# Kernel optimization log

Measured on AMD Instinct MI355X. Metric: run time of the kernel, lower is better.

The kernel has to match this reference:

```python
import jax, jax.numpy as jnp
import numpy as np


def _chain_edges(n):
    # bidirectional chain edges + self loops (PyG GATConv add_self_loops=True default)
    src = np.concatenate([np.arange(n - 1), np.arange(1, n), np.arange(n)])
    dst = np.concatenate([np.arange(1, n), np.arange(n - 1), np.arange(n)])
    return jnp.asarray(src), jnp.asarray(dst)


def _gat(x, W, a_src, a_dst, bias, src, dst, n, heads, ch, concat):
    # x: [B, n, Fin]; PyG GATConv v1 math (lin has no bias, bias added post-agg)
    B = x.shape[0]
    xh = (x @ W).reshape(B, n, heads, ch)  # [B,n,h,c]
    es = jnp.einsum('bnhc,hc->bnh', xh, a_src)
    ed = jnp.einsum('bnhc,hc->bnh', xh, a_dst)
    e = jax.nn.leaky_relu(es[:, src] + ed[:, dst], 0.2)  # [B,E,h]
    e = jnp.moveaxis(e, 1, 0)                            # [E,B,h]
    m = jax.ops.segment_max(e, dst, num_segments=n)      # scatter-softmax over incoming edges
    w = jnp.exp(e - m[dst])
    denom = jax.ops.segment_sum(w, dst, num_segments=n)
    alpha = w / denom[dst]                               # [E,B,h]
    msgs = alpha[..., None] * jnp.moveaxis(xh[:, src], 1, 0)  # [E,B,h,c]
    out = jnp.moveaxis(jax.ops.segment_sum(msgs, dst, num_segments=n), 0, 1)  # [B,n,h,c]
    out = out.reshape(B, n, heads * ch) if concat else out.mean(axis=2)
    return out + bias


def _mlp(x, w1, b1, w2, b2, w3, b3):
    h = jax.nn.leaky_relu(x @ w1 + b1, 0.01)
    h = jax.nn.leaky_relu(h @ w2 + b2, 0.01)
    return h @ w3 + b3


def setup_inputs() -> dict:
    key = jax.random.key(0)
    ks = jax.random.split(key, 21)
    B, n, d_state, hid, da = 2048, 50, 64, 128, 4
    r = lambda k, shp, s: (jax.random.normal(k, shp, dtype=jnp.float32) * s)
    return {
        'state': r(ks[0], (B, n, d_state), 1.0),
        'W1': r(ks[1], (d_state, 2 * hid), 0.1), 'att_src1': r(ks[2], (2, hid), 0.1),
        'att_dst1': r(ks[3], (2, hid), 0.1), 'b1': r(ks[4], (2 * hid,), 0.02),
        'W2': r(ks[5], (2 * hid, hid), 0.1), 'att_src2': r(ks[6], (1, hid), 0.1),
        'att_dst2': r(ks[7], (1, hid), 0.1), 'b2': r(ks[8], (hid,), 0.02),
        'aw1': r(ks[9], (hid, 128), 0.1), 'ab1': r(ks[10], (128,), 0.02),
        'aw2': r(ks[11], (128, 128), 0.1), 'ab2': r(ks[12], (128,), 0.02),
        'aw3': r(ks[13], (128, da), 0.1), 'ab3': r(ks[14], (da,), 0.02),
        'vw1': r(ks[15], (hid, 128), 0.1), 'vb1': r(ks[16], (128,), 0.02),
        'vw2': r(ks[17], (128, 128), 0.1), 'vb2': r(ks[18], (128,), 0.02),
        'vw3': r(ks[19], (128, 1), 0.1), 'vb3': r(ks[20], (1,), 0.02),
    }


def reference(state, W1, att_src1, att_dst1, b1, W2, att_src2, att_dst2, b2,
              aw1, ab1, aw2, ab2, aw3, ab3, vw1, vb1, vw2, vb2, vw3, vb3):
    B, n, _ = state.shape
    src, dst = _chain_edges(n)
    x = jax.nn.gelu(_gat(state, W1, att_src1, att_dst1, b1, src, dst, n, 2, 128, True), approximate=False)
    x = jax.nn.gelu(_gat(x, W2, att_src2, att_dst2, b2, src, dst, n, 1, 128, False), approximate=False)
    graph_emb = x.mean(axis=1)                      # global_mean_pool over chain nodes
    value = _mlp(graph_emb, vw1, vb1, vw2, vb2, vw3, vb3)   # [B,1]
    mean = _mlp(x, aw1, ab1, aw2, ab2, aw3, ab3).reshape(B, -1)  # [B, n*d_action]
    return mean, value
```

## Files before the change

### kernel.cpp

```cpp
#include <hip/hip_runtime.h>

#define DI __device__ __forceinline__

typedef unsigned int uint32;
typedef unsigned short u16;
typedef __attribute__((ext_vector_type(8))) short s8v;
typedef __attribute__((ext_vector_type(4))) float f4v;

DI float lrelu(float x, float s){ return x > 0.f ? x : s*x; }
DI u16 f2bu(float f){ uint32 u = __float_as_uint(f); return (u16)((u + 0x7FFFu + ((u>>16)&1u)) >> 16); }
DI float fastrcp(float x){ float r; asm("v_rcp_f32 %0, %1" : "=v"(r) : "v"(x)); return r; }

DI float gelu_f(float x){
  const float z = fabsf(x) * 0.70710678118654752f;
  const float t = fastrcp(1.f + 0.3275911f*z);
  float p = 1.061405429f;
  p = p*t - 1.453152027f;
  p = p*t + 1.421413741f;
  p = p*t - 0.284496736f;
  p = p*t + 0.254829592f;
  p = p*t;
  const float e = __expf(-z*z);
  float er = 1.f - p*e;
  er = copysignf(er, x);
  return 0.5f*x*(1.f + er);
}

DI f4v mfma16(s8v a, s8v b, f4v c){
  return __builtin_amdgcn_mfma_f32_16x16x32_bf16(a, b, c, 0, 0, 0);
}

constexpr int NNODE = 50;
constexpr int NT = 512;
constexpr int SCS = 134;

constexpr int WS1  = 0;
constexpr int WS2  = 18432;
constexpr int WSA1 = 55296;
constexpr int WSA2 = 71680;
constexpr int WSA3 = 88064;
constexpr int WSTOT= 90112;

__global__ __launch_bounds__(256)
void ac_prep(const float* __restrict__ w1, const float* __restrict__ as1, const float* __restrict__ ad1,
             const float* __restrict__ w2, const float* __restrict__ as2, const float* __restrict__ ad2,
             const float* __restrict__ aw1, const float* __restrict__ aw2, const float* __restrict__ aw3,
             u16* __restrict__ ws)
{
  const int T1 = 2*144*64, T2 = 144*256, T3 = 128*128;
  for (int t = blockIdx.x*blockDim.x + threadIdx.x; t < WSTOT; t += gridDim.x*blockDim.x){
    float v; int o;
    if (t < T1){
      int h = t / 9216, r = t - h*9216, n = r>>6, k = r&63;
      if (n < 128) v = w1[k*256 + h*128 + n];
      else if (n < 130){
        const float* av = ((n==129) ? ad1 : as1) + h*128;
        const float* wr = w1 + k*256 + h*128;
        float s = 0.f;
        for (int c=0;c<128;++c) s += wr[c]*av[c];
        v = s;
      } else v = 0.f;
      o = WS1 + h*9216 + n*64 + k;
    } else if (t < T1+T2){
      int j = t - T1, n = j>>8, k = j&255;
      if (n < 128) v = w2[k*128 + n];
      else if (n < 130){
        const float* av = (n==129) ? ad2 : as2;
        const float* wr = w2 + k*128;
        float s = 0.f;
        for (int c=0;c<128;++c) s += wr[c]*av[c];
        v = s;
      } else v = 0.f;
      o = WS2 + n*256 + k;
    } else if (t < T1+T2+T3){
      int j = t - T1 - T2, n = j>>7, k = j&127;
      v = aw1[k*128 + n];
      o = WSA1 + n*128 + k;
    } else if (t < T1+T2+2*T3){
      int j = t - T1 - T2 - T3, n = j>>7, k = j&127;
      v = aw2[k*128 + n];
      o = WSA2 + n*128 + k;
    } else {
      int j = t - T1 - T2 - 2*T3, m = j>>7, k = j&127;
      v = (m < 4) ? aw3[k*4 + m] : 0.f;
      o = WSA3 + m*128 + k;
    }
    ws[o] = f2bu(v);
  }
}


__global__ __launch_bounds__(NT)
void ac_main(const float* __restrict__ state,
             const float* __restrict__ b1, const float* __restrict__ b2,
             const float* __restrict__ ab1, const float* __restrict__ ab2,
             const float* __restrict__ ab3,
             const float* __restrict__ vw1, const float* __restrict__ vb1,
             const float* __restrict__ vw2, const float* __restrict__ vb2,
             const float* __restrict__ vw3, const float* __restrict__ vb3,
             const u16* __restrict__ ws,
             float* __restrict__ out_mean, float* __restrict__ out_val)
{
  __shared__ __align__(16) float sm[18816];
  float* sc   = sm;
  u16*   pAb  = (u16*)(sm + 8576);
  u16*   pAb2 = pAb + 8192;
  u16*   pAs  = (u16*)(sm + 16768);
  float* geb4 = sm + 16768;
  float* geb  = sm + 17280;
  float* vh1  = sm + 17408;

  const int tid = threadIdx.x, b = blockIdx.x;
  const int wid = tid>>6, l15 = tid&15, g = (tid>>4)&3;

  {
    const float4* xb4 = (const float4*)(state + (size_t)b * (NNODE*64));
    for (int t = tid; t < 800; t += NT){
      float4 v = xb4[t];
      int i = t>>4, k0 = (t&15)*4;
      ushort4 u;
      u.x = f2bu(v.x); u.y = f2bu(v.y); u.z = f2bu(v.z); u.w = f2bu(v.w);
      *(ushort4*)(pAs + i*64 + (k0 ^ ((i&7)<<3))) = u;
    }
    for (int t = tid; t < 224; t += NT){
      int i = 50 + (t>>4), k0 = (t&15)*4;
      *(ushort4*)(pAs + i*64 + (k0 ^ ((i&7)<<3))) = (ushort4){0,0,0,0};
    }
  }
  __syncthreads();

  {
    s8v aS[4][2];
    #pragma unroll
    for (int mt=0;mt<4;++mt)
      #pragma unroll
      for (int ks=0;ks<2;++ks){
        int row = mt*16 + l15, c = ks*32 + g*8;
        aS[mt][ks] = *(const s8v*)(pAs + row*64 + (c ^ ((row&7)<<3)));
      }

    for (int h=0; h<2; ++h){
      for (int nt = wid; nt < 9; nt += 8){
        f4v acc[4];
        #pragma unroll
        for (int mt=0;mt<4;++mt) acc[mt] = (f4v){0.f,0.f,0.f,0.f};
        #pragma unroll
        for (int ks=0;ks<2;++ks){
          s8v bf = *(const s8v*)(ws + WS1 + h*9216 + (nt*16 + l15)*64 + ks*32 + g*8);
          #pragma unroll
          for (int mt=0;mt<4;++mt) acc[mt] = mfma16(aS[mt][ks], bf, acc[mt]);
        }
        const int col = nt*16 + l15;
        if (col < 130){
          #pragma unroll
          for (int mt=0;mt<4;++mt){
            const int r0 = mt*16 + g*4;
            #pragma unroll
            for (int r=0;r<4;++r) sc[(r0+r)*SCS + col] = acc[mt][r];
          }
        }
      }
      __syncthreads();

      {
        const int i = tid & 63;
        if (i < NNODE){
          const float edi = sc[i*SCS + 129];
          const float eS = __expf(lrelu(sc[i*SCS + 128] + edi, 0.2f));
          const float eL = (i > 0)       ? __expf(lrelu(sc[(i-1)*SCS + 128] + edi, 0.2f)) : 0.f;
          const float eR = (i < NNODE-1) ? __expf(lrelu(sc[(i+1)*SCS + 128] + edi, 0.2f)) : 0.f;
          const float rs = fastrcp(eL + eS + eR);
          sc[i*SCS + 130] = eL*rs;
          sc[i*SCS + 131] = eS*rs;
          sc[i*SCS + 132] = eR*rs;
        }
      }
      {
        const int q = tid>>7, j = tid&127, jj = h*128 + j;
        const int i0 = q*13, i1 = (i0+13 < NNODE) ? i0+13 : NNODE;
        const float bj = b1[jj];
        float pv  = (i0 > 0) ? sc[(i0-1)*SCS + j] : 0.f;
        float cur = sc[i0*SCS + j];
        #pragma unroll 4
        for (int i = i0; i < i1; ++i){
          const float nx = (i < NNODE-1) ? sc[(i+1)*SCS + j] : 0.f;
          const float wL = sc[i*SCS + 130], wS = sc[i*SCS + 131], wR = sc[i*SCS + 132];
          const float v = gelu_f(wL*pv + wS*cur + wR*nx + bj);
          pAb[i*256 + (jj ^ ((i&7)<<3))] = f2bu(v);
          pv = cur; cur = nx;
        }
      }
      __syncthreads();
    }
  }

  for (int nt = wid; nt < 9; nt += 8){
    f4v acc[4];
    #pragma unroll
    for (int mt=0;mt<4;++mt) acc[mt] = (f4v){0.f,0.f,0.f,0.f};
    #pragma unroll
    for (int ks=0;ks<8;++ks){
      s8v bf = *(const s8v*)(ws + WS2 + (nt*16 + l15)*256 + ks*32 + g*8);
      #pragma unroll
      for (int mt=0;mt<4;++mt){
        const int row = mt*16 + l15, c = ks*32 + g*8;
        s8v a = *(const s8v*)(pAb + row*256 + (c ^ ((row&7)<<3)));
        acc[mt] = mfma16(a, bf, acc[mt]);
      }
    }
    const int col = nt*16 + l15;
    if (col < 130){
      #pragma unroll
      for (int mt=0;mt<4;++mt){
        const int r0 = mt*16 + g*4;
        #pragma unroll
        for (int r=0;r<4;++r) sc[(r0+r)*SCS + col] = acc[mt][r];
      }
    }
  }
  __syncthreads();

  {
    const int i = tid & 63;
    if (i < NNODE){
      const float edi = sc[i*SCS + 129];
      const float eS = __expf(lrelu(sc[i*SCS + 128] + edi, 0.2f));
      const float eL = (i > 0)       ? __expf(lrelu(sc[(i-1)*SCS + 128] + edi, 0.2f)) : 0.f;
      const float eR = (i < NNODE-1) ? __expf(lrelu(sc[(i+1)*SCS + 128] + edi, 0.2f)) : 0.f;
      const float rs = fastrcp(eL + eS + eR);
      sc[i*SCS + 130] = eL*rs;
      sc[i*SCS + 131] = eS*rs;
      sc[i*SCS + 132] = eR*rs;
    }
  }
  {
    const int q = tid>>7, j = tid&127;
    const int i0 = q*13, i1 = (i0+13 < NNODE) ? i0+13 : NNODE;
    const float bj = b2[j];
    float ps = 0.f;
    float pv  = (i0 > 0) ? sc[(i0-1)*SCS + j] : 0.f;
    float cur = sc[i0*SCS + j];
    #pragma unroll 4
    for (int i = i0; i < i1; ++i){
      const float nx = (i < NNODE-1) ? sc[(i+1)*SCS + j] : 0.f;
      const float wL = sc[i*SCS + 130], wS = sc[i*SCS + 131], wR = sc[i*SCS + 132];
      const float v = gelu_f(wL*pv + wS*cur + wR*nx + bj);
      pAb[i*128 + (j ^ ((i&7)<<3))] = f2bu(v);
      ps += v;
      pv = cur; cur = nx;
    }
    geb4[q*128 + j] = ps;
  }
  __syncthreads();

  {
    const int nt = wid;
    f4v acc[4];
    #pragma unroll
    for (int mt=0;mt<4;++mt) acc[mt] = (f4v){0.f,0.f,0.f,0.f};
    #pragma unroll
    for (int ks=0;ks<4;++ks){
      s8v bf = *(const s8v*)(ws + WSA1 + (nt*16 + l15)*128 + ks*32 + g*8);
      #pragma unroll
      for (int mt=0;mt<4;++mt){
        const int row = mt*16 + l15, c = ks*32 + g*8;
        s8v a = *(const s8v*)(pAb + row*128 + (c ^ ((row&7)<<3)));
        acc[mt] = mfma16(a, bf, acc[mt]);
      }
    }
    const int col = nt*16 + l15;
    const float bj = ab1[col];
    #pragma unroll
    for (int mt=0;mt<4;++mt){
      #pragma unroll
      for (int r=0;r<4;++r){
        const int row = mt*16 + g*4 + r;
        const float v = lrelu(acc[mt][r] + bj, 0.01f);
        pAb2[row*128 + (col ^ ((row&7)<<3))] = f2bu(v);
      }
    }
    if (tid < 128)
      geb[tid] = (geb4[tid] + geb4[128+tid] + geb4[256+tid] + geb4[384+tid]) * 0.02f;
  }
  __syncthreads();

  {
    const int nt = wid;
    f4v acc[4];
    #pragma unroll
    for (int mt=0;mt<4;++mt) acc[mt] = (f4v){0.f,0.f,0.f,0.f};
    #pragma unroll
    for (int ks=0;ks<4;++ks){
      s8v bf = *(const s8v*)(ws + WSA2 + (nt*16 + l15)*128 + ks*32 + g*8);
      #pragma unroll
      for (int mt=0;mt<4;++mt){
        const int row = mt*16 + l15, c = ks*32 + g*8;
        s8v a = *(const s8v*)(pAb2 + row*128 + (c ^ ((row&7)<<3)));
        acc[mt] = mfma16(a, bf, acc[mt]);
      }
    }
    const int col = nt*16 + l15;
    const float bj = ab2[col];
    #pragma unroll
    for (int mt=0;mt<4;++mt){
      #pragma unroll
      for (int r=0;r<4;++r){
        const int row = mt*16 + g*4 + r;
        const float v = lrelu(acc[mt][r] + bj, 0.01f);
        pAb[row*128 + (col ^ ((row&7)<<3))] = f2bu(v);
      }
    }
  }
  __syncthreads();

  if (wid < 4){
    const int mt = wid;
    f4v acc = (f4v){0.f,0.f,0.f,0.f};
    #pragma unroll
    for (int ks=0;ks<4;++ks){
      s8v bf = *(const s8v*)(ws + WSA3 + l15*128 + ks*32 + g*8);
      const int row = mt*16 + l15, c = ks*32 + g*8;
      s8v a = *(const s8v*)(pAb + row*128 + (c ^ ((row&7)<<3)));
      acc = mfma16(a, bf, acc);
    }
    if (l15 < 4){
      const float bj = ab3[l15];
      #pragma unroll
      for (int r=0;r<4;++r){
        const int row = mt*16 + g*4 + r;
        if (row < NNODE) out_mean[(size_t)b*200 + row*4 + l15] = acc[r] + bj;
      }
    }
  } else if (wid == 4){
    const int j = tid & 63;
    float a0=0.f, a1=0.f;
    #pragma unroll 4
    for (int k=0;k<128;++k){
      const float gk = geb[k];
      a0 += gk*vw1[k*128 + j];
      a1 += gk*vw1[k*128 + j + 64];
    }
    vh1[j]      = lrelu(a0 + vb1[j],    0.01f);
    vh1[j + 64] = lrelu(a1 + vb1[j+64], 0.01f);
    asm volatile("s_waitcnt lgkmcnt(0)" ::: "memory");
    __builtin_amdgcn_sched_barrier(0);
    float c0=0.f, c1=0.f;
    #pragma unroll 4
    for (int k=0;k<128;++k){
      const float hk = vh1[k];
      c0 += hk*vw2[k*128 + j];
      c1 += hk*vw2[k*128 + j + 64];
    }
    const float va = lrelu(c0 + vb2[j],    0.01f);
    const float vb = lrelu(c1 + vb2[j+64], 0.01f);
    float p = va*vw3[j] + vb*vw3[j+64];
    #pragma unroll
    for (int off=32; off>0; off>>=1) p += __shfl_down(p, off);
    if (j == 0) out_val[b] = p + vb3[0];
  }
}

extern "C" void kernel_launch(void* const* d_in, const int* in_sizes, int n_in,
                              void* d_out, int out_size, void* d_ws, size_t ws_size,
                              hipStream_t stream)
{
  const float* state = (const float*)d_in[0];
  const float* w1    = (const float*)d_in[1];
  const float* as1   = (const float*)d_in[2];
  const float* ad1   = (const float*)d_in[3];
  const float* b1_   = (const float*)d_in[4];
  const float* w2    = (const float*)d_in[5];
  const float* as2   = (const float*)d_in[6];
  const float* ad2   = (const float*)d_in[7];
  const float* b2_   = (const float*)d_in[8];
  const float* aw1   = (const float*)d_in[9];
  const float* ab1   = (const float*)d_in[10];
  const float* aw2   = (const float*)d_in[11];
  const float* ab2   = (const float*)d_in[12];
  const float* aw3   = (const float*)d_in[13];
  const float* ab3   = (const float*)d_in[14];
  const float* vw1   = (const float*)d_in[15];
  const float* vb1   = (const float*)d_in[16];
  const float* vw2   = (const float*)d_in[17];
  const float* vb2   = (const float*)d_in[18];
  const float* vw3   = (const float*)d_in[19];
  const float* vb3   = (const float*)d_in[20];

  const int B = in_sizes[0] / (NNODE * 64);
  float* out_mean = (float*)d_out;
  float* out_val  = out_mean + (size_t)B * 200;
  u16* ws = (u16*)d_ws;

  ac_prep<<<128, 256, 0, stream>>>(w1, as1, ad1, w2, as2, ad2, aw1, aw2, aw3, ws);
  ac_main<<<B, NT, 0, stream>>>(state, b1_, b2_, ab1, ab2, ab3,
                                vw1, vb1, vw2, vb2, vw3, vb3,
                                ws, out_mean, out_val);
}
```

Baseline: 145.8 us.

## Shrink LDS footprint with bf16 scratch and load inputs directly into MFMA fragments

The fp32 GEMM scratch buffer becomes a bf16 buffer, and the attention scalars and softmax weights move into small separate arrays. This cuts shared memory from about 75KB to about 54KB so more blocks fit per CU, and launch_bounds now asks for 6 waves per SIMD. The state input is loaded from global memory straight into register A-fragments, dropping the LDS staging pass and one barrier. Software bf16 rounding is replaced by the hardware v_cvt_pk_bf16_f32 instruction. Storing the intermediate projections in bf16 adds rounding error before aggregation, and the occupancy hint may raise register pressure.

```diff
diff --git a/kernel.cpp b/kernel.cpp
--- a/kernel.cpp
+++ b/kernel.cpp
@@ -8,8 +8,11 @@
 typedef __attribute__((ext_vector_type(4))) float f4v;
 
 DI float lrelu(float x, float s){ return x > 0.f ? x : s*x; }
+DI float fastrcp(float x){ float r; asm("v_rcp_f32 %0, %1" : "=v"(r) : "v"(x)); return r; }
+DI u16 f2b16(float x){ uint32 r; asm("v_cvt_pk_bf16_f32 %0, %1, %1" : "=v"(r) : "v"(x)); return (u16)r; }
+DI uint32 pk2(float lo, float hi){ uint32 r; asm("v_cvt_pk_bf16_f32 %0, %1, %2" : "=v"(r) : "v"(lo), "v"(hi)); return r; }
+DI float b16f(u16 u){ return __uint_as_float(((uint32)u)<<16); }
 DI u16 f2bu(float f){ uint32 u = __float_as_uint(f); return (u16)((u + 0x7FFFu + ((u>>16)&1u)) >> 16); }
-DI float fastrcp(float x){ float r; asm("v_rcp_f32 %0, %1" : "=v"(r) : "v"(x)); return r; }
 
 DI float gelu_f(float x){
   const float z = fabsf(x) * 0.70710678118654752f;
@@ -32,7 +35,6 @@
 
 constexpr int NNODE = 50;
 constexpr int NT = 512;
-constexpr int SCS = 134;
 
 constexpr int WS1  = 0;
 constexpr int WS2  = 18432;
@@ -90,7 +92,7 @@
 }
 
 
-__global__ __launch_bounds__(NT)
+__global__ __launch_bounds__(NT, 6)
 void ac_main(const float* __restrict__ state,
              const float* __restrict__ b1, const float* __restrict__ b2,
              const float* __restrict__ ab1, const float* __restrict__ ab2,
@@ -101,97 +103,104 @@
              const u16* __restrict__ ws,
              float* __restrict__ out_mean, float* __restrict__ out_val)
 {
-  __shared__ __align__(16) float sm[18816];
-  float* sc   = sm;
-  u16*   pAb  = (u16*)(sm + 8576);
+  __shared__ __align__(16) float sm[13504];
+  u16*   pAb  = (u16*)sm;
   u16*   pAb2 = pAb + 8192;
-  u16*   pAs  = (u16*)(sm + 16768);
-  float* geb4 = sm + 16768;
-  float* geb  = sm + 17280;
-  float* vh1  = sm + 17408;
+  u16*   Cb   = (u16*)(sm + 8192);
+  float* es   = sm + 12416;
+  float* ed   = sm + 12480;
+  float* wLp  = sm + 12544;
+  float* wSp  = sm + 12608;
+  float* wRp  = sm + 12672;
+  float* geb4 = sm + 12736;
+  float* geb  = sm + 13248;
+  float* vh1  = sm + 13376;
 
   const int tid = threadIdx.x, b = blockIdx.x;
   const int wid = tid>>6, l15 = tid&15, g = (tid>>4)&3;
 
+  s8v aS[4][2];
   {
-    const float4* xb4 = (const float4*)(state + (size_t)b * (NNODE*64));
-    for (int t = tid; t < 800; t += NT){
-      float4 v = xb4[t];
-      int i = t>>4, k0 = (t&15)*4;
-      ushort4 u;
-      u.x = f2bu(v.x); u.y = f2bu(v.y); u.z = f2bu(v.z); u.w = f2bu(v.w);
-      *(ushort4*)(pAs + i*64 + (k0 ^ ((i&7)<<3))) = u;
-    }
-    for (int t = tid; t < 224; t += NT){
-      int i = 50 + (t>>4), k0 = (t&15)*4;
-      *(ushort4*)(pAs + i*64 + (k0 ^ ((i&7)<<3))) = (ushort4){0,0,0,0};
-    }
-  }
-  __syncthreads();
-
-  {
-    s8v aS[4][2];
-    #pragma unroll
-    for (int mt=0;mt<4;++mt)
+    const float* xb = state + (size_t)b * (NNODE*64);
+    #pragma unroll
+    for (int mt=0;mt<4;++mt){
+      const int row = mt*16 + l15;
       #pragma unroll
       for (int ks=0;ks<2;++ks){
-        int row = mt*16 + l15, c = ks*32 + g*8;
-        aS[mt][ks] = *(const s8v*)(pAs + row*64 + (c ^ ((row&7)<<3)));
-      }
-
-    for (int h=0; h<2; ++h){
-      for (int nt = wid; nt < 9; nt += 8){
-        f4v acc[4];
-        #pragma unroll
-        for (int mt=0;mt<4;++mt) acc[mt] = (f4v){0.f,0.f,0.f,0.f};
-        #pragma unroll
-        for (int ks=0;ks<2;++ks){
-          s8v bf = *(const s8v*)(ws + WS1 + h*9216 + (nt*16 + l15)*64 + ks*32 + g*8);
+        union { s8v v; uint32 u[4]; } fr;
+        if (row < NNODE){
+          const float4 f0 = *(const float4*)(xb + row*64 + ks*32 + g*8);
+          const float4 f1 = *(const float4*)(xb + row*64 + ks*32 + g*8 + 4);
+          fr.u[0] = pk2(f0.x, f0.y); fr.u[1] = pk2(f0.z, f0.w);
+          fr.u[2] = pk2(f1.x, f1.y); fr.u[3] = pk2(f1.z, f1.w);
+        } else {
+          fr.u[0] = fr.u[1] = fr.u[2] = fr.u[3] = 0u;
+        }
+        aS[mt][ks] = fr.v;
+      }
+    }
+  }
+
+  for (int h=0; h<2; ++h){
+    for (int nt = wid; nt < 9; nt += 8){
+      f4v acc[4];
+      #pragma unroll
+      for (int mt=0;mt<4;++mt) acc[mt] = (f4v){0.f,0.f,0.f,0.f};
+      #pragma unroll
+      for (int ks=0;ks<2;++ks){
+        s8v bf = *(const s8v*)(ws + WS1 + h*9216 + (nt*16 + l15)*64 + ks*32 + g*8);
+        #pragma unroll
+        for (int mt=0;mt<4;++mt) acc[mt] = mfma16(aS[mt][ks], bf, acc[mt]);
+      }
+      const int col = nt*16 + l15;
+      if (col < 128){
+        #pragma unroll
+        for (int mt=0;mt<4;++mt)
           #pragma unroll
-          for (int mt=0;mt<4;++mt) acc[mt] = mfma16(aS[mt][ks], bf, acc[mt]);
-        }
-        const int col = nt*16 + l15;
-        if (col < 130){
+          for (int r=0;r<4;++r){
+            const int row = mt*16 + g*4 + r;
+            Cb[row*132 + col] = f2b16(acc[mt][r]);
+          }
+      } else if (col == 128){
+        #pragma unroll
+        for (int mt=0;mt<4;++mt)
           #pragma unroll
-          for (int mt=0;mt<4;++mt){
-            const int r0 = mt*16 + g*4;
-            #pragma unroll
-            for (int r=0;r<4;++r) sc[(r0+r)*SCS + col] = acc[mt][r];
-          }
-        }
-      }
-      __syncthreads();
-
-      {
-        const int i = tid & 63;
-        if (i < NNODE){
-          const float edi = sc[i*SCS + 129];
-          const float eS = __expf(lrelu(sc[i*SCS + 128] + edi, 0.2f));
-          const float eL = (i > 0)       ? __expf(lrelu(sc[(i-1)*SCS + 128] + edi, 0.2f)) : 0.f;
-          const float eR = (i < NNODE-1) ? __expf(lrelu(sc[(i+1)*SCS + 128] + edi, 0.2f)) : 0.f;
-          const float rs = fastrcp(eL + eS + eR);
-          sc[i*SCS + 130] = eL*rs;
-          sc[i*SCS + 131] = eS*rs;
-          sc[i*SCS + 132] = eR*rs;
-        }
-      }
-      {
-        const int q = tid>>7, j = tid&127, jj = h*128 + j;
-        const int i0 = q*13, i1 = (i0+13 < NNODE) ? i0+13 : NNODE;
-        const float bj = b1[jj];
-        float pv  = (i0 > 0) ? sc[(i0-1)*SCS + j] : 0.f;
-        float cur = sc[i0*SCS + j];
-        #pragma unroll 4
-        for (int i = i0; i < i1; ++i){
-          const float nx = (i < NNODE-1) ? sc[(i+1)*SCS + j] : 0.f;
-          const float wL = sc[i*SCS + 130], wS = sc[i*SCS + 131], wR = sc[i*SCS + 132];
-          const float v = gelu_f(wL*pv + wS*cur + wR*nx + bj);
-          pAb[i*256 + (jj ^ ((i&7)<<3))] = f2bu(v);
-          pv = cur; cur = nx;
-        }
-      }
-      __syncthreads();
-    }
+          for (int r=0;r<4;++r) es[mt*16 + g*4 + r] = acc[mt][r];
+      } else if (col == 129){
+        #pragma unroll
+        for (int mt=0;mt<4;++mt)
+          #pragma unroll
+          for (int r=0;r<4;++r) ed[mt*16 + g*4 + r] = acc[mt][r];
+      }
+    }
+    __syncthreads();
+
+    {
+      const int i = tid & 63;
+      if (i < NNODE){
+        const float edi = ed[i];
+        const float eS = __expf(lrelu(es[i] + edi, 0.2f));
+        const float eL = (i > 0)       ? __expf(lrelu(es[i-1] + edi, 0.2f)) : 0.f;
+        const float eR = (i < NNODE-1) ? __expf(lrelu(es[i+1] + edi, 0.2f)) : 0.f;
+        const float rs = fastrcp(eL + eS + eR);
+        wLp[i] = eL*rs; wSp[i] = eS*rs; wRp[i] = eR*rs;
+      }
+    }
+    {
+      const int q = tid>>7, j = tid&127, jj = h*128 + j;
+      const int i0 = q*13, i1 = (i0+13 < NNODE) ? i0+13 : NNODE;
+      const float bj = b1[jj];
+      float pv  = (i0 > 0) ? b16f(Cb[(i0-1)*132 + j]) : 0.f;
+      float cur = b16f(Cb[i0*132 + j]);
+      #pragma unroll 4
+      for (int i = i0; i < i1; ++i){
+        const float nx = (i < NNODE-1) ? b16f(Cb[(i+1)*132 + j]) : 0.f;
+        const float v = gelu_f(wLp[i]*pv + wSp[i]*cur + wRp[i]*nx + bj);
+        pAb[i*256 + (jj ^ ((i&7)<<3))] = f2b16(v);
+        pv = cur; cur = nx;
+      }
+    }
+    __syncthreads();
   }
 
   for (int nt = wid; nt < 9; nt += 8){
@@ -209,13 +218,24 @@
       }
     }
     const int col = nt*16 + l15;
-    if (col < 130){
-      #pragma unroll
-      for (int mt=0;mt<4;++mt){
-        const int r0 = mt*16 + g*4;
-        #pragma unroll
-        for (int r=0;r<4;++r) sc[(r0+r)*SCS + col] = acc[mt][r];
-      }
+    if (col < 128){
+      #pragma unroll
+      for (int mt=0;mt<4;++mt)
+        #pragma unroll
+        for (int r=0;r<4;++r){
+          const int row = mt*16 + g*4 + r;
+          Cb[row*132 + col] = f2b16(acc[mt][r]);
+        }
+    } else if (col == 128){
+      #pragma unroll
+      for (int mt=0;mt<4;++mt)
+        #pragma unroll
+        for (int r=0;r<4;++r) es[mt*16 + g*4 + r] = acc[mt][r];
+    } else if (col == 129){
+      #pragma unroll
+      for (int mt=0;mt<4;++mt)
+        #pragma unroll
+        for (int r=0;r<4;++r) ed[mt*16 + g*4 + r] = acc[mt][r];
     }
   }
   __syncthreads();
@@ -223,14 +243,12 @@
   {
     const int i = tid & 63;
     if (i < NNODE){
-      const float edi = sc[i*SCS + 129];
-      const float eS = __expf(lrelu(sc[i*SCS + 128] + edi, 0.2f));
-      const float eL = (i > 0)       ? __expf(lrelu(sc[(i-1)*SCS + 128] + edi, 0.2f)) : 0.f;
-      const float eR = (i < NNODE-1) ? __expf(lrelu(sc[(i+1)*SCS + 128] + edi, 0.2f)) : 0.f;
+      const float edi = ed[i];
+      const float eS = __expf(lrelu(es[i] + edi, 0.2f));
+      const float eL = (i > 0)       ? __expf(lrelu(es[i-1] + edi, 0.2f)) : 0.f;
+      const float eR = (i < NNODE-1) ? __expf(lrelu(es[i+1] + edi, 0.2f)) : 0.f;
       const float rs = fastrcp(eL + eS + eR);
-      sc[i*SCS + 130] = eL*rs;
-      sc[i*SCS + 131] = eS*rs;
-      sc[i*SCS + 132] = eR*rs;
+      wLp[i] = eL*rs; wSp[i] = eS*rs; wRp[i] = eR*rs;
     }
   }
   {
@@ -238,14 +256,13 @@
     const int i0 = q*13, i1 = (i0+13 < NNODE) ? i0+13 : NNODE;
     const float bj = b2[j];
     float ps = 0.f;
-    float pv  = (i0 > 0) ? sc[(i0-1)*SCS + j] : 0.f;
-    float cur = sc[i0*SCS + j];
+    float pv  = (i0 > 0) ? b16f(Cb[(i0-1)*132 + j]) : 0.f;
+    float cur = b16f(Cb[i0*132 + j]);
     #pragma unroll 4
     for (int i = i0; i < i1; ++i){
-      const float nx = (i < NNODE-1) ? sc[(i+1)*SCS + j] : 0.f;
-      const float wL = sc[i*SCS + 130], wS = sc[i*SCS + 131], wR = sc[i*SCS + 132];
-      const float v = gelu_f(wL*pv + wS*cur + wR*nx + bj);
-      pAb[i*128 + (j ^ ((i&7)<<3))] = f2bu(v);
+      const float nx = (i < NNODE-1) ? b16f(Cb[(i+1)*132 + j]) : 0.f;
+      const float v = gelu_f(wLp[i]*pv + wSp[i]*cur + wRp[i]*nx + bj);
+      pAb[i*128 + (j ^ ((i&7)<<3))] = f2b16(v);
       ps += v;
       pv = cur; cur = nx;
     }
@@ -276,7 +293,7 @@
       for (int r=0;r<4;++r){
         const int row = mt*16 + g*4 + r;
         const float v = lrelu(acc[mt][r] + bj, 0.01f);
-        pAb2[row*128 + (col ^ ((row&7)<<3))] = f2bu(v);
+        pAb2[row*128 + (col ^ ((row&7)<<3))] = f2b16(v);
       }
     }
     if (tid < 128)
@@ -307,7 +324,7 @@
       for (int r=0;r<4;++r){
         const int row = mt*16 + g*4 + r;
         const float v = lrelu(acc[mt][r] + bj, 0.01f);
-        pAb[row*128 + (col ^ ((row&7)<<3))] = f2bu(v);
+        pAb[row*128 + (col ^ ((row&7)<<3))] = f2b16(v);
       }
     }
   }
```

New measurement: 225.4 us. +54.6%, slower.
